# Performance work log

Hardware: AMD Instinct MI355X
Metric: run time of the kernel (lower is better)

The kernel has to match this reference:

```python
import jax, jax.numpy as jnp
import numpy as np

N, E, Q = 50000, 500000, 100000
IN_DIM, HID, EDGE_DIM, NUM_CLASSES = 128, 128, 16, 2


def _glorot(key, shape):
    fan_in, fan_out = shape
    lim = (6.0 / (fan_in + fan_out)) ** 0.5
    return jax.random.uniform(key, shape, jnp.float32, -lim, lim)


def setup_inputs() -> dict:
    key = jax.random.key(0)
    ks = jax.random.split(key, 12)
    return {
        "node_feature": jax.random.normal(ks[0], (N, IN_DIM), jnp.float32),
        "edge_index": jax.random.randint(ks[1], (2, E), 0, N, jnp.int64),
        "edge_feature": jax.random.normal(ks[2], (E, EDGE_DIM), jnp.float32),
        "edge_label_index": jax.random.randint(ks[3], (2, Q), 0, N, jnp.int64),
        # conv1 params
        "c1_pre_W": _glorot(ks[4], (IN_DIM, IN_DIM)),
        "c1_pre_b": jnp.zeros((IN_DIM,), jnp.float32),
        "c1_msg_W": _glorot(ks[5], (2 * IN_DIM + EDGE_DIM, HID)),
        "c1_msg_b": jnp.zeros((HID,), jnp.float32),
        # conv2 params
        "c2_pre_W": _glorot(ks[6], (HID, HID)),
        "c2_pre_b": jnp.zeros((HID,), jnp.float32),
        "c2_msg_W": _glorot(ks[7], (2 * HID + EDGE_DIM, HID)),
        "c2_msg_b": jnp.zeros((HID,), jnp.float32),
        # link-prediction head
        "lp_W": _glorot(ks[8], (2 * HID, NUM_CLASSES)),
        "lp_b": jnp.zeros((NUM_CLASSES,), jnp.float32),
    }


def _mlp_message_conv(x, edge_index, edge_feature, pre_W, pre_b, msg_W, msg_b):
    # pre_conv: Linear + ReLU
    h = jax.nn.relu(x @ pre_W + pre_b)
    src, dst = edge_index[0], edge_index[1]
    # PyG default flow source_to_target: x_i = target, x_j = source
    x_i = h[dst]  # [E, d]
    x_j = h[src]  # [E, d]
    msg = jnp.concatenate([x_i, x_j, edge_feature], axis=1) @ msg_W + msg_b  # [E, out]
    # aggr='add' onto target nodes
    return jax.ops.segment_sum(msg, dst, num_segments=x.shape[0])


def reference(node_feature, edge_index, edge_feature, edge_label_index,
              c1_pre_W, c1_pre_b, c1_msg_W, c1_msg_b,
              c2_pre_W, c2_pre_b, c2_msg_W, c2_msg_b,
              lp_W, lp_b):
    # eval mode: dropout is identity
    x = jax.nn.relu(_mlp_message_conv(node_feature, edge_index, edge_feature,
                                      c1_pre_W, c1_pre_b, c1_msg_W, c1_msg_b))
    x = _mlp_message_conv(x, edge_index, edge_feature,
                          c2_pre_W, c2_pre_b, c2_msg_W, c2_msg_b)
    nodes_first = x[edge_label_index[0]]   # [Q, hid]
    nodes_second = x[edge_label_index[1]]  # [Q, hid]
    pred = jnp.concatenate([nodes_first, nodes_second], axis=-1) @ lp_W + lp_b
    return pred
```

## Files before the change

kernel.cpp:

```cpp
#include <hip/hip_runtime.h>
#include <cstdint>
#include <cstddef>


typedef __attribute__((ext_vector_type(8))) short short8;
typedef __attribute__((ext_vector_type(4))) float float4v;

__device__ __forceinline__ ushort f2b(float f) {
    uint u = __float_as_uint(f);
    u = u + 0x7fff + ((u >> 16) & 1);
    return (ushort)(u >> 16);
}
__device__ __forceinline__ float b2f(ushort h) {
    return __uint_as_float(((uint)h) << 16);
}
__device__ __forceinline__ uint pack2(float a, float b) {
    return (uint)f2b(a) | ((uint)f2b(b) << 16);
}

#define F_MSG     1
#define F_RELU    2
#define F_DEGBIAS 4
#define F_OUTB    8
#define F_IN32    16
#define F_HEAD    32

#define XS_STRIDE 72

__launch_bounds__(256, 2)
__global__ void gemm_mfma(const ushort* __restrict__ A, const ushort* __restrict__ B,
                          const ushort* __restrict__ EF, const float* __restrict__ A32,
                          const float* __restrict__ DEG, const ushort* __restrict__ Wt,
                          const float* __restrict__ bias, ushort* __restrict__ outB,
                          const float* __restrict__ lpW, float* __restrict__ z,
                          int M, int Kp, int flags)
{
    __shared__ ushort xs[128 * XS_STRIDE];
    __shared__ ushort ws[128 * XS_STRIDE];
    const int tid  = threadIdx.x;
    const int lane = tid & 63;
    const int wave = tid >> 6;
    const int row0 = blockIdx.x << 7;

    float4v acc[2][8];
#pragma unroll
    for (int m = 0; m < 2; ++m)
#pragma unroll
        for (int t = 0; t < 8; ++t) acc[m][t] = (float4v){0.f, 0.f, 0.f, 0.f};

    const int arow0 = (wave << 5) + (lane & 15);
    const int koff  = (lane >> 4) << 3;
    const int bcol  = lane & 15;

    for (int kt = 0; kt < Kp; kt += 64) {
        __syncthreads();
        for (int idx = tid; idx < 128 * 8; idx += 256) {
            const int n = idx >> 3;
            const int g = idx & 7;
            const uint4 v = *(const uint4*)&Wt[(size_t)n * Kp + kt + (g << 3)];
            *(uint4*)&ws[n * XS_STRIDE + (g << 3)] = v;
        }
        if (flags & F_MSG) {
            for (int idx = tid; idx < 128 * 8; idx += 256) {
                const int r  = idx >> 3;
                const int g  = idx & 7;
                const int gr = row0 + r;
                const int kk = kt + (g << 3);
                uint4 v = make_uint4(0, 0, 0, 0);
                if (gr < M) {
                    if (kk < 128) {
                        uint4 a = *(const uint4*)&A[((size_t)gr << 7) + kk];
                        const float d = DEG[gr];
                        uint* p = (uint*)&a;
#pragma unroll
                        for (int q = 0; q < 4; ++q)
                            p[q] = pack2(b2f((ushort)(p[q] & 0xffff)) * d,
                                         b2f((ushort)(p[q] >> 16)) * d);
                        v = a;
                    } else if (kk < 256) {
                        v = *(const uint4*)&B[((size_t)gr << 7) + kk - 128];
                    } else if (kk < 272) {
                        v = *(const uint4*)&EF[((size_t)gr << 4) + kk - 256];
                    }
                }
                *(uint4*)&xs[r * XS_STRIDE + (g << 3)] = v;
            }
        } else if (flags & F_IN32) {
            for (int idx = tid; idx < 128 * 8; idx += 256) {
                const int r  = idx >> 3;
                const int g  = idx & 7;
                const int gr = row0 + r;
                uint4 v = make_uint4(0, 0, 0, 0);
                if (gr < M) {
                    const float4 f0 = *(const float4*)&A32[((size_t)gr << 7) + kt + (g << 3)];
                    const float4 f1 = *(const float4*)&A32[((size_t)gr << 7) + kt + (g << 3) + 4];
                    v.x = pack2(f0.x, f0.y); v.y = pack2(f0.z, f0.w);
                    v.z = pack2(f1.x, f1.y); v.w = pack2(f1.z, f1.w);
                }
                *(uint4*)&xs[r * XS_STRIDE + (g << 3)] = v;
            }
        } else {
            for (int idx = tid; idx < 128 * 8; idx += 256) {
                const int r  = idx >> 3;
                const int g  = idx & 7;
                const int gr = row0 + r;
                uint4 v = make_uint4(0, 0, 0, 0);
                if (gr < M) v = *(const uint4*)&A[((size_t)gr << 7) + kt + (g << 3)];
                *(uint4*)&xs[r * XS_STRIDE + (g << 3)] = v;
            }
        }
        __syncthreads();
#pragma unroll
        for (int s = 0; s < 64; s += 32) {
            const short8 a0 = *(const short8*)&xs[arow0 * XS_STRIDE + s + koff];
            const short8 a1 = *(const short8*)&xs[(arow0 + 16) * XS_STRIDE + s + koff];
#pragma unroll
            for (int t = 0; t < 8; ++t) {
                const short8 bf = *(const short8*)&ws[((t << 4) + bcol) * XS_STRIDE + s + koff];
                acc[0][t] = __builtin_amdgcn_mfma_f32_16x16x32_bf16(a0, bf, acc[0][t], 0, 0, 0);
                acc[1][t] = __builtin_amdgcn_mfma_f32_16x16x32_bf16(a1, bf, acc[1][t], 0, 0, 0);
            }
        }
    }

    float bcv[8];
#pragma unroll
    for (int t = 0; t < 8; ++t) bcv[t] = bias[(t << 4) + bcol];

    if (flags & F_HEAD) {
        const float2* lw = (const float2*)lpW;
        float2 wa[8], wb[8];
#pragma unroll
        for (int t = 0; t < 8; ++t) {
            const int col = (t << 4) + bcol;
            wa[t] = lw[col];
            wb[t] = lw[128 + col];
        }
#pragma unroll
        for (int m = 0; m < 2; ++m) {
            const int rbase = row0 + (wave << 5) + (m << 4) + ((lane >> 4) << 2);
#pragma unroll
            for (int r = 0; r < 4; ++r) {
                const int row = rbase + r;
                const float d = (row < M) ? DEG[row] : 0.f;
                float za0 = 0.f, za1 = 0.f, zb0 = 0.f, zb1 = 0.f;
#pragma unroll
                for (int t = 0; t < 8; ++t) {
                    const float v = acc[m][t][r] + d * bcv[t];
                    za0 += v * wa[t].x; za1 += v * wa[t].y;
                    zb0 += v * wb[t].x; zb1 += v * wb[t].y;
                }
#pragma unroll
                for (int mk = 8; mk > 0; mk >>= 1) {
                    za0 += __shfl_xor(za0, mk);
                    za1 += __shfl_xor(za1, mk);
                    zb0 += __shfl_xor(zb0, mk);
                    zb1 += __shfl_xor(zb1, mk);
                }
                if (bcol == 0 && row < M)
                    *(float4*)&z[(size_t)row * 4] = make_float4(za0, za1, zb0, zb1);
            }
        }
    } else {
#pragma unroll
        for (int m = 0; m < 2; ++m) {
            const int rbase = row0 + (wave << 5) + (m << 4) + ((lane >> 4) << 2);
#pragma unroll
            for (int t = 0; t < 8; ++t) {
                const int col = (t << 4) + bcol;
#pragma unroll
                for (int r = 0; r < 4; ++r) {
                    const int row = rbase + r;
                    if (row >= M) continue;
                    float v = acc[m][t][r];
                    v += (flags & F_DEGBIAS) ? DEG[row] * bcv[t] : bcv[t];
                    if (flags & F_RELU) v = fmaxf(v, 0.f);
                    outB[((size_t)row << 7) + col] = f2b(v);
                }
            }
        }
    }
}

__launch_bounds__(256)
__global__ void prep(const float* __restrict__ c1pW, const float* __restrict__ c2pW,
                     const float* __restrict__ c1mW, const float* __restrict__ c2mW,
                     ushort* __restrict__ wtp1, ushort* __restrict__ wtp2,
                     ushort* __restrict__ wtm1, ushort* __restrict__ wtm2,
                     int* __restrict__ counts, int N)
{
    const int gtid = blockIdx.x * 256 + threadIdx.x;
    const int gstr = gridDim.x * 256;
    for (int i = gtid; i < N; i += gstr) counts[i] = 0;
    for (int idx = gtid; idx < 128 * 128; idx += gstr) {
        const int n = idx >> 7, k = idx & 127;
        wtp1[idx] = f2b(c1pW[(size_t)k * 128 + n]);
        wtp2[idx] = f2b(c2pW[(size_t)k * 128 + n]);
    }
    for (int idx = gtid; idx < 128 * 320; idx += gstr) {
        const int n = idx / 320, k = idx - n * 320;
        wtm1[idx] = (k < 272) ? f2b(c1mW[(size_t)k * 128 + n]) : (ushort)0;
        wtm2[idx] = (k < 272) ? f2b(c2mW[(size_t)k * 128 + n]) : (ushort)0;
    }
}

__launch_bounds__(256)
__global__ void hist_kernel(const int* __restrict__ ei, int* __restrict__ counts, int E)
{
    const int e = blockIdx.x * 256 + threadIdx.x;
    if (e < E) atomicAdd(&counts[ei[E + e]], 1);
}

__launch_bounds__(256)
__global__ void scan_phase1(const int* __restrict__ counts, int* __restrict__ rowstart,
                            int* __restrict__ blocksums, int N)
{
    __shared__ int sdata[256];
    const int t = threadIdx.x;
    const int i = blockIdx.x * 256 + t;
    const int v = (i < N) ? counts[i] : 0;
    sdata[t] = v;
    __syncthreads();
    for (int off = 1; off < 256; off <<= 1) {
        const int add = (t >= off) ? sdata[t - off] : 0;
        __syncthreads();
        sdata[t] += add;
        __syncthreads();
    }
    if (i < N) rowstart[i] = sdata[t] - v;
    if (t == 255) blocksums[blockIdx.x] = sdata[255];
}

__launch_bounds__(256)
__global__ void scan_phase23(const int* __restrict__ counts, const int* __restrict__ bs,
                             int* __restrict__ rowstart, int* __restrict__ cursor,
                             float* __restrict__ degf, int N, int E)
{
    __shared__ int sdata[256];
    const int t = threadIdx.x;
    const int vb = blockIdx.x;
    int part = 0;
    for (int j = t; j < vb; j += 256) part += bs[j];
    sdata[t] = part;
    __syncthreads();
    for (int s = 128; s > 0; s >>= 1) {
        if (t < s) sdata[t] += sdata[t + s];
        __syncthreads();
    }
    const int off = sdata[0];
    const int i = vb * 256 + t;
    if (i < N) {
        const int rs = rowstart[i] + off;
        rowstart[i] = rs;
        cursor[i]   = rs;
        degf[i]     = (float)counts[i];
    }
    if (vb == 0 && t == 0) rowstart[N] = E;
}

__launch_bounds__(256)
__global__ void build_elist(const int* __restrict__ ei, int* __restrict__ cursor,
                            int2* __restrict__ elist, int E)
{
    const int e = blockIdx.x * 256 + threadIdx.x;
    if (e >= E) return;
    const int d = ei[E + e];
    const int pos = atomicAdd(&cursor[d], 1);
    elist[pos] = make_int2(ei[e], e);
}

__launch_bounds__(256)
__global__ void gather(const int2* __restrict__ elist, const int* __restrict__ rowstart,
                       const ushort* __restrict__ h, ushort* __restrict__ agg,
                       const float* __restrict__ ef, ushort* __restrict__ aggef,
                       int N, int doEf)
{
    const int tid = threadIdx.x;
    const int grp = tid >> 4;
    const int l   = tid & 15;
    const int nvb = (N + 15) / 16;
    for (int vb = blockIdx.x; vb < nvb; vb += gridDim.x) {
        const int node = vb * 16 + grp;
        if (node >= N) continue;
        const int beg = rowstart[node];
        const int end = rowstart[node + 1];
        float a0 = 0.f, a1 = 0.f, a2 = 0.f, a3 = 0.f;
        float a4 = 0.f, a5 = 0.f, a6 = 0.f, a7 = 0.f;
        float efacc = 0.f;
        int k = beg;
        while (k < end) {
            const int cnt = min(16, end - k);
            const int2 ep = elist[k + min(l, cnt - 1)];
            int j = 0;
            for (; j + 8 <= cnt; j += 8) {
                uint4 v[8];
                float efv[8];
#pragma unroll
                for (int jj = 0; jj < 8; ++jj) {
                    const int s = __shfl(ep.x, j + jj, 16);
                    v[jj] = *(const uint4*)&h[((size_t)s << 7) + (l << 3)];
                    if (doEf) {
                        const int y = __shfl(ep.y, j + jj, 16);
                        efv[jj] = ef[((size_t)y << 4) + l];
                    }
                }
#pragma unroll
                for (int jj = 0; jj < 8; ++jj) {
                    a0 += b2f((ushort)(v[jj].x & 0xffff));
                    a1 += b2f((ushort)(v[jj].x >> 16));
                    a2 += b2f((ushort)(v[jj].y & 0xffff));
                    a3 += b2f((ushort)(v[jj].y >> 16));
                    a4 += b2f((ushort)(v[jj].z & 0xffff));
                    a5 += b2f((ushort)(v[jj].z >> 16));
                    a6 += b2f((ushort)(v[jj].w & 0xffff));
                    a7 += b2f((ushort)(v[jj].w >> 16));
                    if (doEf) efacc += efv[jj];
                }
            }
            for (; j < cnt; ++j) {
                const int s = __shfl(ep.x, j, 16);
                const uint4 v = *(const uint4*)&h[((size_t)s << 7) + (l << 3)];
                if (doEf) {
                    const int y = __shfl(ep.y, j, 16);
                    efacc += ef[((size_t)y << 4) + l];
                }
                a0 += b2f((ushort)(v.x & 0xffff));
                a1 += b2f((ushort)(v.x >> 16));
                a2 += b2f((ushort)(v.y & 0xffff));
                a3 += b2f((ushort)(v.y >> 16));
                a4 += b2f((ushort)(v.z & 0xffff));
                a5 += b2f((ushort)(v.z >> 16));
                a6 += b2f((ushort)(v.w & 0xffff));
                a7 += b2f((ushort)(v.w >> 16));
            }
            k += cnt;
        }
        uint4 o;
        o.x = pack2(a0, a1);
        o.y = pack2(a2, a3);
        o.z = pack2(a4, a5);
        o.w = pack2(a6, a7);
        *(uint4*)&agg[((size_t)node << 7) + (l << 3)] = o;
        if (doEf) aggef[((size_t)node << 4) + l] = f2b(efacc);
    }
}

__launch_bounds__(256)
__global__ void head_kernel(const float4* __restrict__ z, const int* __restrict__ eli,
                            const float* __restrict__ lpb, float* __restrict__ out, int Q)
{
    const int q = blockIdx.x * 256 + threadIdx.x;
    if (q >= Q) return;
    const int a = eli[q];
    const int b = eli[Q + q];
    const float4 za = z[a];
    const float4 zb = z[b];
    float2 o = make_float2(za.x + zb.z + lpb[0], za.y + zb.w + lpb[1]);
    *(float2*)&out[(size_t)q * 2] = o;
}

extern "C" void kernel_launch(void* const* d_in, const int* in_sizes, int n_in,
                              void* d_out, int out_size, void* d_ws, size_t ws_size,
                              hipStream_t stream)
{
    const float* nf   = (const float*)d_in[0];
    const int*   ei   = (const int*)d_in[1];
    const float* ef   = (const float*)d_in[2];
    const int*   eli  = (const int*)d_in[3];
    const float* c1pW = (const float*)d_in[4];
    const float* c1pb = (const float*)d_in[5];
    const float* c1mW = (const float*)d_in[6];
    const float* c1mb = (const float*)d_in[7];
    const float* c2pW = (const float*)d_in[8];
    const float* c2pb = (const float*)d_in[9];
    const float* c2mW = (const float*)d_in[10];
    const float* c2mb = (const float*)d_in[11];
    const float* lpW  = (const float*)d_in[12];
    const float* lpb  = (const float*)d_in[13];
    float* out = (float*)d_out;

    const int N = in_sizes[0] / 128;
    const int E = in_sizes[1] / 2;
    const int Q = in_sizes[3] / 2;

    float* DEG = (float*)d_ws;
    float* z   = DEG + N;
    int* counts    = (int*)(z + (size_t)N * 4);
    int* rowstart  = counts + N;
    int* cursor    = rowstart + N + 1;
    int* blocksums = cursor + N;
    uintptr_t ep8 = (uintptr_t)(blocksums + 1024);
    ep8 = (ep8 + 7) & ~(uintptr_t)7;
    int2* elist = (int2*)ep8;
    uintptr_t up = (uintptr_t)(elist + E);
    up = (up + 15) & ~(uintptr_t)15;
    ushort* h_bf   = (ushort*)up;
    ushort* agg_bf = h_bf   + (size_t)N * 128;
    ushort* x1_bf  = agg_bf + (size_t)N * 128;
    ushort* ef_bf  = x1_bf  + (size_t)N * 128;
    ushort* wtp1   = ef_bf  + (size_t)N * 16;
    ushort* wtm1   = wtp1 + 128 * 128;
    ushort* wtp2   = wtm1 + 128 * 320;
    ushort* wtm2   = wtp2 + 128 * 128;

    const int gemmGrid = (N + 127) / 128;
    const int eGrid    = (E + 255) / 256;
    const int nGrid    = (N + 255) / 256;
    const int gGrid    = (N + 15) / 16;
    const int headGrid = (Q + 255) / 256;

    prep<<<nGrid, 256, 0, stream>>>(c1pW, c2pW, c1mW, c2mW, wtp1, wtp2, wtm1, wtm2,
                                    counts, N);
    hist_kernel<<<eGrid, 256, 0, stream>>>(ei, counts, E);
    scan_phase1<<<nGrid, 256, 0, stream>>>(counts, rowstart, blocksums, N);
    scan_phase23<<<nGrid, 256, 0, stream>>>(counts, blocksums, rowstart, cursor, DEG, N, E);
    build_elist<<<eGrid, 256, 0, stream>>>(ei, cursor, elist, E);

    gemm_mfma<<<gemmGrid, 256, 0, stream>>>(nullptr, nullptr, nullptr, nf, DEG, wtp1,
                                            c1pb, h_bf, nullptr, nullptr, N, 128,
                                            F_RELU | F_OUTB | F_IN32);
    gather<<<gGrid, 256, 0, stream>>>(elist, rowstart, h_bf, agg_bf, ef, ef_bf, N, 1);
    gemm_mfma<<<gemmGrid, 256, 0, stream>>>(h_bf, agg_bf, ef_bf, nullptr, DEG, wtm1,
                                            c1mb, x1_bf, nullptr, nullptr, N, 320,
                                            F_MSG | F_RELU | F_DEGBIAS | F_OUTB);

    gemm_mfma<<<gemmGrid, 256, 0, stream>>>(x1_bf, nullptr, nullptr, nullptr, DEG, wtp2,
                                            c2pb, h_bf, nullptr, nullptr, N, 128,
                                            F_RELU | F_OUTB);
    gather<<<gGrid, 256, 0, stream>>>(elist, rowstart, h_bf, agg_bf, nullptr, nullptr, N, 0);
    gemm_mfma<<<gemmGrid, 256, 0, stream>>>(h_bf, agg_bf, ef_bf, nullptr, DEG, wtm2,
                                            c2mb, nullptr, lpW, z, N, 320,
                                            F_MSG | F_DEGBIAS | F_HEAD);

    head_kernel<<<headGrid, 256, 0, stream>>>((const float4*)z, eli, lpb, out, Q);
}
```

Measured before the change: 316.7 us.

## Load GEMM tiles via global_load_lds with XOR-swizzled LDS and pre-scaled inputs

The GEMM kernel now stages weight and activation tiles with direct global-to-LDS loads instead of register round-trips. The LDS layout changes from padded rows to an XOR swizzle, and the weights are pre-swizzled in prep to match. The degree-scaled copy of h is now written in the preceding GEMM epilogue (outD), which removes the per-tile bf16 unpack, scale and repack in the message GEMM. Edge features are padded to 64 columns so every K tile is a uniform 128-byte row copy. Launch bounds rise to 3 blocks per CU. The cost is an extra N×128 output write, a padded edge-feature buffer that prep must zero, and a second rounding step in the pre-scaled bf16 values.

```diff
diff --git a/kernel.cpp b/kernel.cpp
--- a/kernel.cpp
+++ b/kernel.cpp
@@ -16,6 +16,12 @@
 }
 __device__ __forceinline__ uint pack2(float a, float b) {
     return (uint)f2b(a) | ((uint)f2b(b) << 16);
+}
+
+__device__ __forceinline__ void gload16(const void* gsrc, void* ldst) {
+    __builtin_amdgcn_global_load_lds(
+        (const __attribute__((address_space(1))) void*)gsrc,
+        (__attribute__((address_space(3))) void*)ldst, 16, 0, 0);
 }
 
 #define F_MSG     1
@@ -25,18 +31,17 @@
 #define F_IN32    16
 #define F_HEAD    32
 
-#define XS_STRIDE 72
-
-__launch_bounds__(256, 2)
+__launch_bounds__(256, 3)
 __global__ void gemm_mfma(const ushort* __restrict__ A, const ushort* __restrict__ B,
                           const ushort* __restrict__ EF, const float* __restrict__ A32,
                           const float* __restrict__ DEG, const ushort* __restrict__ Wt,
                           const float* __restrict__ bias, ushort* __restrict__ outB,
+                          ushort* __restrict__ outD,
                           const float* __restrict__ lpW, float* __restrict__ z,
                           int M, int Kp, int flags)
 {
-    __shared__ ushort xs[128 * XS_STRIDE];
-    __shared__ ushort ws[128 * XS_STRIDE];
+    __shared__ ushort xs[128 * 64];
+    __shared__ ushort ws[128 * 64];
     const int tid  = threadIdx.x;
     const int lane = tid & 63;
     const int wave = tid >> 6;
@@ -48,75 +53,61 @@
 #pragma unroll
         for (int t = 0; t < 8; ++t) acc[m][t] = (float4v){0.f, 0.f, 0.f, 0.f};
 
-    const int arow0 = (wave << 5) + (lane & 15);
-    const int koff  = (lane >> 4) << 3;
+    const int ar0   = (wave << 5) + (lane & 15);
     const int bcol  = lane & 15;
+    const int cxor  = lane & 7;
+    const int koffc = lane >> 4;
+    const int sw16  = (((lane & 7) ^ (lane >> 3)) << 4);
 
     for (int kt = 0; kt < Kp; kt += 64) {
+        const int tix = kt >> 6;
         __syncthreads();
-        for (int idx = tid; idx < 128 * 8; idx += 256) {
-            const int n = idx >> 3;
-            const int g = idx & 7;
-            const uint4 v = *(const uint4*)&Wt[(size_t)n * Kp + kt + (g << 3)];
-            *(uint4*)&ws[n * XS_STRIDE + (g << 3)] = v;
-        }
-        if (flags & F_MSG) {
+#pragma unroll
+        for (int i = 0; i < 4; ++i) {
+            const int wsoff = (wave << 11) + (i << 9);
+            gload16((const char*)Wt + (((size_t)((tix << 13) + wsoff)) << 1) + (lane << 4),
+                    &ws[wsoff]);
+        }
+        if (flags & F_IN32) {
             for (int idx = tid; idx < 128 * 8; idx += 256) {
                 const int r  = idx >> 3;
-                const int g  = idx & 7;
-                const int gr = row0 + r;
-                const int kk = kt + (g << 3);
-                uint4 v = make_uint4(0, 0, 0, 0);
-                if (gr < M) {
-                    if (kk < 128) {
-                        uint4 a = *(const uint4*)&A[((size_t)gr << 7) + kk];
-                        const float d = DEG[gr];
-                        uint* p = (uint*)&a;
-#pragma unroll
-                        for (int q = 0; q < 4; ++q)
-                            p[q] = pack2(b2f((ushort)(p[q] & 0xffff)) * d,
-                                         b2f((ushort)(p[q] >> 16)) * d);
-                        v = a;
-                    } else if (kk < 256) {
-                        v = *(const uint4*)&B[((size_t)gr << 7) + kk - 128];
-                    } else if (kk < 272) {
-                        v = *(const uint4*)&EF[((size_t)gr << 4) + kk - 256];
-                    }
-                }
-                *(uint4*)&xs[r * XS_STRIDE + (g << 3)] = v;
-            }
-        } else if (flags & F_IN32) {
-            for (int idx = tid; idx < 128 * 8; idx += 256) {
-                const int r  = idx >> 3;
-                const int g  = idx & 7;
+                const int ch = idx & 7;
                 const int gr = row0 + r;
                 uint4 v = make_uint4(0, 0, 0, 0);
                 if (gr < M) {
-                    const float4 f0 = *(const float4*)&A32[((size_t)gr << 7) + kt + (g << 3)];
-                    const float4 f1 = *(const float4*)&A32[((size_t)gr << 7) + kt + (g << 3) + 4];
+                    const float4 f0 = *(const float4*)&A32[((size_t)gr << 7) + kt + (ch << 3)];
+                    const float4 f1 = *(const float4*)&A32[((size_t)gr << 7) + kt + (ch << 3) + 4];
                     v.x = pack2(f0.x, f0.y); v.y = pack2(f0.z, f0.w);
                     v.z = pack2(f1.x, f1.y); v.w = pack2(f1.z, f1.w);
                 }
-                *(uint4*)&xs[r * XS_STRIDE + (g << 3)] = v;
+                *(uint4*)&xs[(r << 6) + ((ch ^ (r & 7)) << 3)] = v;
             }
         } else {
-            for (int idx = tid; idx < 128 * 8; idx += 256) {
-                const int r  = idx >> 3;
-                const int g  = idx & 7;
-                const int gr = row0 + r;
-                uint4 v = make_uint4(0, 0, 0, 0);
-                if (gr < M) v = *(const uint4*)&A[((size_t)gr << 7) + kt + (g << 3)];
-                *(uint4*)&xs[r * XS_STRIDE + (g << 3)] = v;
+            const char* srcB; size_t strideB; int toffB;
+            if (flags & F_MSG) {
+                if (tix < 2)      { srcB = (const char*)A;  strideB = 256; toffB = (tix & 1) << 7; }
+                else if (tix < 4) { srcB = (const char*)B;  strideB = 256; toffB = (tix & 1) << 7; }
+                else              { srcB = (const char*)EF; strideB = 128; toffB = 0; }
+            } else {
+                srcB = (const char*)A; strideB = 256; toffB = (tix & 1) << 7;
+            }
+            const int rb = wave << 5;
+#pragma unroll
+            for (int i = 0; i < 4; ++i) {
+                const int gr = min(row0 + rb + (i << 3) + (lane >> 3), M - 1);
+                gload16(srcB + (size_t)gr * strideB + toffB + sw16,
+                        &xs[(rb + (i << 3)) << 6]);
             }
         }
         __syncthreads();
 #pragma unroll
-        for (int s = 0; s < 64; s += 32) {
-            const short8 a0 = *(const short8*)&xs[arow0 * XS_STRIDE + s + koff];
-            const short8 a1 = *(const short8*)&xs[(arow0 + 16) * XS_STRIDE + s + koff];
+        for (int sc = 0; sc < 8; sc += 4) {
+            const int ra = (sc + koffc) ^ cxor;
+            const short8 a0 = *(const short8*)&xs[(ar0 << 6) + (ra << 3)];
+            const short8 a1 = *(const short8*)&xs[((ar0 + 16) << 6) + (ra << 3)];
 #pragma unroll
             for (int t = 0; t < 8; ++t) {
-                const short8 bf = *(const short8*)&ws[((t << 4) + bcol) * XS_STRIDE + s + koff];
+                const short8 bf = *(const short8*)&ws[(((t << 4) + bcol) << 6) + (ra << 3)];
                 acc[0][t] = __builtin_amdgcn_mfma_f32_16x16x32_bf16(a0, bf, acc[0][t], 0, 0, 0);
                 acc[1][t] = __builtin_amdgcn_mfma_f32_16x16x32_bf16(a1, bf, acc[1][t], 0, 0, 0);
             }
@@ -166,16 +157,18 @@
         for (int m = 0; m < 2; ++m) {
             const int rbase = row0 + (wave << 5) + (m << 4) + ((lane >> 4) << 2);
 #pragma unroll
-            for (int t = 0; t < 8; ++t) {
-                const int col = (t << 4) + bcol;
-#pragma unroll
-                for (int r = 0; r < 4; ++r) {
-                    const int row = rbase + r;
-                    if (row >= M) continue;
+            for (int r = 0; r < 4; ++r) {
+                const int row = rbase + r;
+                if (row >= M) continue;
+                const float d = DEG[row];
+#pragma unroll
+                for (int t = 0; t < 8; ++t) {
+                    const int col = (t << 4) + bcol;
                     float v = acc[m][t][r];
-                    v += (flags & F_DEGBIAS) ? DEG[row] * bcv[t] : bcv[t];
+                    v += (flags & F_DEGBIAS) ? d * bcv[t] : bcv[t];
                     if (flags & F_RELU) v = fmaxf(v, 0.f);
                     outB[((size_t)row << 7) + col] = f2b(v);
+                    if (outD) outD[((size_t)row << 7) + col] = f2b(v * d);
                 }
             }
         }
@@ -187,18 +180,22 @@
                      const float* __restrict__ c1mW, const float* __restrict__ c2mW,
                      ushort* __restrict__ wtp1, ushort* __restrict__ wtp2,
                      ushort* __restrict__ wtm1, ushort* __restrict__ wtm2,
-                     int* __restrict__ counts, int N)
+                     ushort* __restrict__ efp, int* __restrict__ counts, int N)
 {
     const int gtid = blockIdx.x * 256 + threadIdx.x;
     const int gstr = gridDim.x * 256;
     for (int i = gtid; i < N; i += gstr) counts[i] = 0;
-    for (int idx = gtid; idx < 128 * 128; idx += gstr) {
-        const int n = idx >> 7, k = idx & 127;
+    for (int i = gtid; i < N * 8; i += gstr)
+        ((uint4*)efp)[i] = make_uint4(0, 0, 0, 0);
+    for (int idx = gtid; idx < 2 * 128 * 64; idx += gstr) {
+        const int s = idx & 63, n = (idx >> 6) & 127, t = idx >> 13;
+        const int k = t * 64 + (((s >> 3) ^ (n & 7)) << 3) + (s & 7);
         wtp1[idx] = f2b(c1pW[(size_t)k * 128 + n]);
         wtp2[idx] = f2b(c2pW[(size_t)k * 128 + n]);
     }
-    for (int idx = gtid; idx < 128 * 320; idx += gstr) {
-        const int n = idx / 320, k = idx - n * 320;
+    for (int idx = gtid; idx < 5 * 128 * 64; idx += gstr) {
+        const int s = idx & 63, n = (idx >> 6) & 127, t = idx >> 13;
+        const int k = t * 64 + (((s >> 3) ^ (n & 7)) << 3) + (s & 7);
         wtm1[idx] = (k < 272) ? f2b(c1mW[(size_t)k * 128 + n]) : (ushort)0;
         wtm2[idx] = (k < 272) ? f2b(c2mW[(size_t)k * 128 + n]) : (ushort)0;
     }
@@ -341,7 +338,7 @@
         o.z = pack2(a4, a5);
         o.w = pack2(a6, a7);
         *(uint4*)&agg[((size_t)node << 7) + (l << 3)] = o;
-        if (doEf) aggef[((size_t)node << 4) + l] = f2b(efacc);
+        if (doEf) aggef[((size_t)node << 6) + l] = f2b(efacc);
     }
 }
 
@@ -397,11 +394,12 @@
     ushort* h_bf   = (ushort*)up;
     ushort* agg_bf = h_bf   + (size_t)N * 128;
     ushort* x1_bf  = agg_bf + (size_t)N * 128;
-    ushort* ef_bf  = x1_bf  + (size_t)N * 128;
-    ushort* wtp1   = ef_bf  + (size_t)N * 16;
-    ushort* wtm1   = wtp1 + 128 * 128;
-    ushort* wtp2   = wtm1 + 128 * 320;
-    ushort* wtm2   = wtp2 + 128 * 128;
+    ushort* hd_bf  = x1_bf  + (size_t)N * 128;
+    ushort* efp    = hd_bf  + (size_t)N * 128;
+    ushort* wtp1   = efp    + (size_t)N * 64;
+    ushort* wtm1   = wtp1 + 2 * 128 * 64;
+    ushort* wtp2   = wtm1 + 5 * 128 * 64;
+    ushort* wtm2   = wtp2 + 2 * 128 * 64;
 
     const int gemmGrid = (N + 127) / 128;
     const int eGrid    = (E + 255) / 256;
@@ -410,26 +408,26 @@
     const int headGrid = (Q + 255) / 256;
 
     prep<<<nGrid, 256, 0, stream>>>(c1pW, c2pW, c1mW, c2mW, wtp1, wtp2, wtm1, wtm2,
-                                    counts, N);
+                                    efp, counts, N);
     hist_kernel<<<eGrid, 256, 0, stream>>>(ei, counts, E);
     scan_phase1<<<nGrid, 256, 0, stream>>>(counts, rowstart, blocksums, N);
     scan_phase23<<<nGrid, 256, 0, stream>>>(counts, blocksums, rowstart, cursor, DEG, N, E);
     build_elist<<<eGrid, 256, 0, stream>>>(ei, cursor, elist, E);
 
     gemm_mfma<<<gemmGrid, 256, 0, stream>>>(nullptr, nullptr, nullptr, nf, DEG, wtp1,
-                                            c1pb, h_bf, nullptr, nullptr, N, 128,
+                                            c1pb, h_bf, hd_bf, nullptr, nullptr, N, 128,
                                             F_RELU | F_OUTB | F_IN32);
-    gather<<<gGrid, 256, 0, stream>>>(elist, rowstart, h_bf, agg_bf, ef, ef_bf, N, 1);
-    gemm_mfma<<<gemmGrid, 256, 0, stream>>>(h_bf, agg_bf, ef_bf, nullptr, DEG, wtm1,
-                                            c1mb, x1_bf, nullptr, nullptr, N, 320,
+    gather<<<gGrid, 256, 0, stream>>>(elist, rowstart, h_bf, agg_bf, ef, efp, N, 1);
+    gemm_mfma<<<gemmGrid, 256, 0, stream>>>(hd_bf, agg_bf, efp, nullptr, DEG, wtm1,
+                                            c1mb, x1_bf, nullptr, nullptr, nullptr, N, 320,
                                             F_MSG | F_RELU | F_DEGBIAS | F_OUTB);
 
     gemm_mfma<<<gemmGrid, 256, 0, stream>>>(x1_bf, nullptr, nullptr, nullptr, DEG, wtp2,
-                                            c2pb, h_bf, nullptr, nullptr, N, 128,
+                                            c2pb, h_bf, hd_bf, nullptr, nullptr, N, 128,
                                             F_RELU | F_OUTB);
     gather<<<gGrid, 256, 0, stream>>>(elist, rowstart, h_bf, agg_bf, nullptr, nullptr, N, 0);
-    gemm_mfma<<<gemmGrid, 256, 0, stream>>>(h_bf, agg_bf, ef_bf, nullptr, DEG, wtm2,
-                                            c2mb, nullptr, lpW, z, N, 320,
+    gemm_mfma<<<gemmGrid, 256, 0, stream>>>(hd_bf, agg_bf, efp, nullptr, DEG, wtm2,
+                                            c2mb, nullptr, nullptr, lpW, z, N, 320,
                                             F_MSG | F_DEGBIAS | F_HEAD);
 
     head_kernel<<<headGrid, 256, 0, stream>>>((const float4*)z, eli, lpb, out, Q);
```

New measurement: 291.8 us. 1.09x faster.
